# Optimization experiments

Measured on AMD Instinct MI355X. Metric: run time of the kernel, lower is better.

## Reference

```python
import jax, jax.numpy as jnp
import numpy as np

C, B, N, IN, OUT = 10, 128, 1152, 8, 16  # num_capsules, batch, num_route_nodes, in_ch, out_ch
NUM_ITERS = 3


def squash(t):
    # t: [..., OUT]
    sq_norm = jnp.sum(t * t, axis=-1, keepdims=True)
    scale = sq_norm / (1.0 + sq_norm)
    return scale * t / jnp.sqrt(sq_norm + 1e-8)


def setup_inputs() -> dict:
    key = jax.random.key(0)
    k1, k2 = jax.random.split(key)
    x = jax.random.normal(k1, (B, N, IN), dtype=jnp.float32)
    route_weights = jax.random.normal(k2, (C, N, IN, OUT), dtype=jnp.float32)
    return {"x": x, "route_weights": route_weights}


def reference(x, route_weights):
    # priors[c,b,n,o] = sum_i x[b,n,i] * W[c,n,i,o]
    priors = jnp.einsum('bni,cnio->cbno', x, route_weights)  # [C,B,N,OUT]
    # torch: logits = zeros_like(priors[:, :, :, 0]) -> [C,B,N,OUT] (dim 3 was the
    # singleton matmul row dim, so the OUT axis survives on the logits)
    logits = jnp.zeros_like(priors)
    outputs = None
    for _ in range(NUM_ITERS):
        attn = jax.nn.softmax(logits, axis=2)            # over route nodes N
        outputs = squash(jnp.sum(attn * priors, axis=2))  # [C,B,OUT]
        # (outputs * priors).sum(-1) broadcasts to [C,B,N,1] added to [C,B,N,OUT]
        logits = logits + jnp.sum(outputs[:, :, None, :] * priors, axis=-1, keepdims=True)
    return outputs  # [C,B,OUT] == outputs.squeeze() in torch (B>1, C>1)
```

## Files before the change

### kernel.cpp

```cpp
#include <hip/hip_runtime.h>
#include <hip/hip_bf16.h>


constexpr int C = 10, B = 128, N = 1152, IN = 8, OUT = 16;

__device__ __forceinline__ unsigned packbf(float a, float b) {
    __hip_bfloat162 h = __float22bfloat162_rn(float2{a, b});
    return *(unsigned*)&h;
}
__device__ __forceinline__ float bflo(unsigned u) { return __uint_as_float(u << 16); }
__device__ __forceinline__ float bfhi(unsigned u) { return __uint_as_float(u & 0xffff0000u); }

constexpr int T1 = 512;
constexpr int BT = 16;

__global__ __launch_bounds__(T1)
void priors_gemm(const float* __restrict__ Xf, const float* __restrict__ Wf,
                 uint2* __restrict__ Pws) {
    const int t = threadIdx.x;
    const int l = t & 63;
    const int wid = t >> 6;
    const int q = l & 3;
    const int rsub = l >> 2;
    const int blk = blockIdx.x;
    const int bt = blk & 7;
    const int rest = blk >> 3;
    const int nc = rest % 9;
    const int c = rest / 9;
    const int n = nc * 128 + wid * 16 + rsub;

    const float4* wr = (const float4*)(Wf + (size_t)(c * N + n) * (IN * OUT));
    float4 wv[IN];
    #pragma unroll
    for (int i = 0; i < IN; ++i) wv[i] = wr[i * 4 + q];

    #pragma unroll 4
    for (int g = 0; g < BT; ++g) {
        const int b = bt * BT + g;
        const float4* xr = (const float4*)(Xf + (size_t)(b * N + n) * IN);
        const float4 xa = xr[0], xc = xr[1];
        const float xs[8] = { xa.x, xa.y, xa.z, xa.w, xc.x, xc.y, xc.z, xc.w };
        float a0 = 0.f, a1 = 0.f, a2 = 0.f, a3 = 0.f;
        #pragma unroll
        for (int i = 0; i < IN; ++i) {
            a0 = fmaf(xs[i], wv[i].x, a0);
            a1 = fmaf(xs[i], wv[i].y, a1);
            a2 = fmaf(xs[i], wv[i].z, a2);
            a3 = fmaf(xs[i], wv[i].w, a3);
        }
        Pws[((size_t)(c * B + b) * N + n) * 4 + q] =
            uint2{packbf(a0, a1), packbf(a2, a3)};
    }
}

constexpr int T2 = 512;
constexpr int NW2 = T2 / 64;
constexpr int PASSES = N / (NW2 * 16);

__global__ __launch_bounds__(T2)
void routing(const uint2* __restrict__ Pws, float* __restrict__ Of) {
    __shared__ uint2 ldsP[N * 4];
    __shared__ float lds_s[NW2][OUT];
    __shared__ float lds_sum[NW2];
    __shared__ float lds_out[OUT];

    const int t = threadIdx.x;
    const int l = t & 63;
    const int wid = t >> 6;
    const int q = l & 3;
    const int rsub = l >> 2;
    const int blk = blockIdx.x;

    const uint2* src = Pws + (size_t)blk * (N * 4);
    #pragma unroll
    for (int k = 0; k < (N * 4) / T2; ++k)
        ldsP[k * T2 + t] = src[k * T2 + t];
    __syncthreads();

    float oa[4] = {0.f, 0.f, 0.f, 0.f};

    for (int it = 0; it < 3; ++it) {
        float s0 = 0.f, s1 = 0.f, s2 = 0.f, s3 = 0.f, ssum = 0.f;
        if (it == 0) {
            ssum = (float)PASSES;
            #pragma unroll
            for (int p = 0; p < PASSES; ++p) {
                const int n = wid * (16 * PASSES) + p * 16 + rsub;
                const uint2 u = ldsP[n * 4 + q];
                s0 += bflo(u.x); s1 += bfhi(u.x);
                s2 += bflo(u.y); s3 += bfhi(u.y);
            }
        } else {
            #pragma unroll
            for (int p = 0; p < PASSES; ++p) {
                const int n = wid * (16 * PASSES) + p * 16 + rsub;
                const uint2 u = ldsP[n * 4 + q];
                const float p0 = bflo(u.x), p1 = bfhi(u.x);
                const float p2 = bflo(u.y), p3 = bfhi(u.y);
                float d = oa[0] * p0;
                d = fmaf(oa[1], p1, d);
                d = fmaf(oa[2], p2, d);
                d = fmaf(oa[3], p3, d);
                d += __shfl_xor(d, 1, 64);
                d += __shfl_xor(d, 2, 64);
                const float e = __expf(d);
                ssum += e;
                s0 = fmaf(e, p0, s0);
                s1 = fmaf(e, p1, s1);
                s2 = fmaf(e, p2, s2);
                s3 = fmaf(e, p3, s3);
            }
        }
        #pragma unroll
        for (int m = 4; m < 64; m <<= 1) {
            ssum += __shfl_xor(ssum, m, 64);
            s0 += __shfl_xor(s0, m, 64);
            s1 += __shfl_xor(s1, m, 64);
            s2 += __shfl_xor(s2, m, 64);
            s3 += __shfl_xor(s3, m, 64);
        }
        if (l < 4) {
            lds_s[wid][l * 4 + 0] = s0;
            lds_s[wid][l * 4 + 1] = s1;
            lds_s[wid][l * 4 + 2] = s2;
            lds_s[wid][l * 4 + 3] = s3;
        }
        if (l == 0) lds_sum[wid] = ssum;
        __syncthreads();

        if (t < OUT) {
            float so = 0.f, S = 0.f;
            #pragma unroll
            for (int w = 0; w < NW2; ++w) { so += lds_s[w][t]; S += lds_sum[w]; }
            so /= S;
            float r = so * so;
            r += __shfl_xor(r, 1, 64);
            r += __shfl_xor(r, 2, 64);
            r += __shfl_xor(r, 4, 64);
            r += __shfl_xor(r, 8, 64);
            const float ov = so * (r / ((1.f + r) * sqrtf(r + 1e-8f)));
            if (it == 2) Of[(size_t)blk * OUT + t] = ov;
            else         lds_out[t] = ov;
        }

        if (it < 2) {
            __syncthreads();
            oa[0] += lds_out[q * 4 + 0];
            oa[1] += lds_out[q * 4 + 1];
            oa[2] += lds_out[q * 4 + 2];
            oa[3] += lds_out[q * 4 + 3];
        }
    }
}

extern "C" void kernel_launch(void* const* d_in, const int* in_sizes, int n_in,
                              void* d_out, int out_size, void* d_ws, size_t ws_size,
                              hipStream_t stream) {
    const float* X = (const float*)d_in[0];
    const float* W = (const float*)d_in[1];
    float* O = (float*)d_out;
    uint2* P = (uint2*)d_ws;

    hipLaunchKernelGGL(priors_gemm, dim3(C * 9 * 8), dim3(T1), 0, stream, X, W, P);
    hipLaunchKernelGGL(routing, dim3(C * B), dim3(T2), 0, stream, P, O);
}
```

Measured before the change: 96.28 us.

## Fuse priors GEMM into routing kernel, computing priors straight into LDS

Merges the two kernels into one. Each (capsule, batch) block now computes its priors from X and W directly into shared memory instead of writing bf16 priors to a global workspace and reading them back. This removes the workspace round trip and one launch. In exchange, each block re-reads its capsule's full W slice (W is reloaded once per batch element, 128x more W traffic, mostly served from cache), and the first iteration now sums fp32 priors rather than bf16-rounded ones.

```diff
diff --git a/kernel.cpp b/kernel.cpp
--- a/kernel.cpp
+++ b/kernel.cpp
@@ -3,6 +3,9 @@
 
 
 constexpr int C = 10, B = 128, N = 1152, IN = 8, OUT = 16;
+constexpr int THREADS = 512;
+constexpr int NW = THREADS / 64;
+constexpr int PASSES = N / (NW * 16);
 
 __device__ __forceinline__ unsigned packbf(float a, float b) {
     __hip_bfloat162 h = __float22bfloat162_rn(float2{a, b});
@@ -11,32 +14,32 @@
 __device__ __forceinline__ float bflo(unsigned u) { return __uint_as_float(u << 16); }
 __device__ __forceinline__ float bfhi(unsigned u) { return __uint_as_float(u & 0xffff0000u); }
 
-constexpr int T1 = 512;
-constexpr int BT = 16;
+__global__ __launch_bounds__(THREADS)
+void caps_route(const float* __restrict__ Xf, const float* __restrict__ Wf,
+                float* __restrict__ Of) {
+    __shared__ uint2 ldsP[PASSES * THREADS];
+    __shared__ float lds_s[NW][OUT];
+    __shared__ float lds_sum[NW];
+    __shared__ float lds_out[OUT];
 
-__global__ __launch_bounds__(T1)
-void priors_gemm(const float* __restrict__ Xf, const float* __restrict__ Wf,
-                 uint2* __restrict__ Pws) {
     const int t = threadIdx.x;
     const int l = t & 63;
     const int wid = t >> 6;
     const int q = l & 3;
     const int rsub = l >> 2;
     const int blk = blockIdx.x;
-    const int bt = blk & 7;
-    const int rest = blk >> 3;
-    const int nc = rest % 9;
-    const int c = rest / 9;
-    const int n = nc * 128 + wid * 16 + rsub;
+    const int c = blk >> 7;
+    const int b = blk & 127;
 
-    const float4* wr = (const float4*)(Wf + (size_t)(c * N + n) * (IN * OUT));
-    float4 wv[IN];
+    float s0 = 0.f, s1 = 0.f, s2 = 0.f, s3 = 0.f;
+
     #pragma unroll
-    for (int i = 0; i < IN; ++i) wv[i] = wr[i * 4 + q];
-
-    #pragma unroll 4
-    for (int g = 0; g < BT; ++g) {
-        const int b = bt * BT + g;
+    for (int p = 0; p < PASSES; ++p) {
+        const int n = wid * (16 * PASSES) + p * 16 + rsub;
+        const float4* wr = (const float4*)(Wf + (size_t)(c * N + n) * (IN * OUT));
+        float4 wv[IN];
+        #pragma unroll
+        for (int i = 0; i < IN; ++i) wv[i] = wr[i * 4 + q];
         const float4* xr = (const float4*)(Xf + (size_t)(b * N + n) * IN);
         const float4 xa = xr[0], xc = xr[1];
         const float xs[8] = { xa.x, xa.y, xa.z, xa.w, xc.x, xc.y, xc.z, xc.w };
@@ -48,53 +51,22 @@
             a2 = fmaf(xs[i], wv[i].z, a2);
             a3 = fmaf(xs[i], wv[i].w, a3);
         }
-        Pws[((size_t)(c * B + b) * N + n) * 4 + q] =
-            uint2{packbf(a0, a1), packbf(a2, a3)};
+        ldsP[p * THREADS + t] = uint2{packbf(a0, a1), packbf(a2, a3)};
+        s0 += a0; s1 += a1; s2 += a2; s3 += a3;
     }
-}
-
-constexpr int T2 = 512;
-constexpr int NW2 = T2 / 64;
-constexpr int PASSES = N / (NW2 * 16);
-
-__global__ __launch_bounds__(T2)
-void routing(const uint2* __restrict__ Pws, float* __restrict__ Of) {
-    __shared__ uint2 ldsP[N * 4];
-    __shared__ float lds_s[NW2][OUT];
-    __shared__ float lds_sum[NW2];
-    __shared__ float lds_out[OUT];
-
-    const int t = threadIdx.x;
-    const int l = t & 63;
-    const int wid = t >> 6;
-    const int q = l & 3;
-    const int rsub = l >> 2;
-    const int blk = blockIdx.x;
-
-    const uint2* src = Pws + (size_t)blk * (N * 4);
-    #pragma unroll
-    for (int k = 0; k < (N * 4) / T2; ++k)
-        ldsP[k * T2 + t] = src[k * T2 + t];
-    __syncthreads();
 
     float oa[4] = {0.f, 0.f, 0.f, 0.f};
 
     for (int it = 0; it < 3; ++it) {
-        float s0 = 0.f, s1 = 0.f, s2 = 0.f, s3 = 0.f, ssum = 0.f;
+        float ssum;
         if (it == 0) {
             ssum = (float)PASSES;
+        } else {
+            ssum = 0.f;
+            s0 = s1 = s2 = s3 = 0.f;
             #pragma unroll
             for (int p = 0; p < PASSES; ++p) {
-                const int n = wid * (16 * PASSES) + p * 16 + rsub;
-                const uint2 u = ldsP[n * 4 + q];
-                s0 += bflo(u.x); s1 += bfhi(u.x);
-                s2 += bflo(u.y); s3 += bfhi(u.y);
-            }
-        } else {
-            #pragma unroll
-            for (int p = 0; p < PASSES; ++p) {
-                const int n = wid * (16 * PASSES) + p * 16 + rsub;
-                const uint2 u = ldsP[n * 4 + q];
+                const uint2 u = ldsP[p * THREADS + t];
                 const float p0 = bflo(u.x), p1 = bfhi(u.x);
                 const float p2 = bflo(u.y), p3 = bfhi(u.y);
                 float d = oa[0] * p0;
@@ -131,7 +103,7 @@
         if (t < OUT) {
             float so = 0.f, S = 0.f;
             #pragma unroll
-            for (int w = 0; w < NW2; ++w) { so += lds_s[w][t]; S += lds_sum[w]; }
+            for (int w = 0; w < NW; ++w) { so += lds_s[w][t]; S += lds_sum[w]; }
             so /= S;
             float r = so * so;
             r += __shfl_xor(r, 1, 64);
@@ -159,8 +131,5 @@
     const float* X = (const float*)d_in[0];
     const float* W = (const float*)d_in[1];
     float* O = (float*)d_out;
-    uint2* P = (uint2*)d_ws;
-
-    hipLaunchKernelGGL(priors_gemm, dim3(C * 9 * 8), dim3(T1), 0, stream, X, W, P);
-    hipLaunchKernelGGL(routing, dim3(C * B), dim3(T2), 0, stream, P, O);
+    hipLaunchKernelGGL(caps_route, dim3(C * B), dim3(THREADS), 0, stream, X, W, O);
 }
```

Measured after the change: 97.48 us. No clear change (+1.2%).
